# Optimization experiments

Measured on AMD Instinct MI355X. Metric: run time of the kernel, lower is better.

The kernel has to match this reference:

```python
import jax, jax.numpy as jnp
import numpy as np

B, NV, NL, D, H = 32, 512, 256, 1024, 4096


def _ffn(x, w1, b1, w2, b2):
    # torch FFN: linear2(relu(linear1(x))); weights stored as [in, out]
    return jnp.maximum(x @ w1 + b1, 0.0) @ w2 + b2


def setup_inputs() -> dict:
    key = jax.random.key(0)
    ks = jax.random.split(key, 12)
    s_in = 1.0 / np.sqrt(D)
    s_h = 1.0 / np.sqrt(H)
    return {
        "V": jax.random.normal(ks[0], (B, NV, D), jnp.float32),
        "L": jax.random.normal(ks[1], (B, NL, D), jnp.float32),
        "v_mask": jnp.ones((B, NV), jnp.float32),
        "l_mask": jnp.ones((B, NL), jnp.float32),
        "w1_V": jax.random.normal(ks[2], (D, H), jnp.float32) * s_in,
        "b1_V": jnp.zeros((H,), jnp.float32),
        "w2_V": jax.random.normal(ks[3], (H, D), jnp.float32) * s_h,
        "b2_V": jnp.zeros((D,), jnp.float32),
        "w1_L": jax.random.normal(ks[4], (D, H), jnp.float32) * s_in,
        "b1_L": jnp.zeros((H,), jnp.float32),
        "w2_L": jax.random.normal(ks[5], (H, D), jnp.float32) * s_h,
        "b2_L": jnp.zeros((D,), jnp.float32),
    }


def reference(V, L, v_mask, l_mask, w1_V, b1_V, w2_V, b2_V, w1_L, b1_L, w2_L, b2_L):
    # masks are unused in the original forward
    fV_V = _ffn(V, w1_V, b1_V, w2_V, b2_V)  # [B, NV, D] = ffn_V(V)
    fL_L = _ffn(L, w1_L, b1_L, w2_L, b2_L)  # [B, NL, D] = ffn_L(L)
    fL_V = _ffn(V, w1_L, b1_L, w2_L, b2_L)  # [B, NV, D] = ffn_L(V) (as in source)
    scale = 1.0 / jnp.sqrt(jnp.asarray(V.shape[-1], V.dtype))
    A_LV = jnp.einsum('bnd,bmd->bnm', fV_V, fL_L) * scale  # [B, NV, NL]
    A_VV = jnp.einsum('bnd,bmd->bnm', fV_V, fL_V) * scale  # [B, NV, NV]
    A = jnp.concatenate([A_LV, A_VV], axis=-1)             # [B, NV, NL+NV]
    # softmax over dim=1 (rows), as in the source
    attn = jax.nn.softmax(A, axis=1)
    KV = jnp.concatenate([fL_L, fV_V], axis=1)              # [B, NL+NV, D]
    V_next = jnp.einsum('bnk,bkd->bnd', attn, KV)           # [B, NV, D]
    return (A, V_next)
```

## Files before the change

kernel.cpp:

```cpp
#include <hip/hip_runtime.h>
#include <stdint.h>

#define B_   32
#define NV_  512
#define NL_  256
#define D_   1024
#define H_   4096
#define KTOT 768
#define SCALE_ 0.03125f

typedef __attribute__((ext_vector_type(8))) __bf16 bf8_t;
typedef __attribute__((ext_vector_type(4))) float f32x4;

__device__ __forceinline__ unsigned short f2bf(float f) {
    unsigned u = __float_as_uint(f);
    u += 0x7FFFu + ((u >> 16) & 1u);
    return (unsigned short)(u >> 16);
}
__device__ __forceinline__ unsigned pk2(float lo, float hi) {
    return (unsigned)f2bf(lo) | ((unsigned)f2bf(hi) << 16);
}

__device__ __forceinline__ void gl_lds16(const void* g, const void* lds) {
    __builtin_amdgcn_global_load_lds(
        (const __attribute__((address_space(1))) unsigned int*)(uintptr_t)g,
        (__attribute__((address_space(3))) unsigned int*)(unsigned)(uintptr_t)lds,
        16, 0, 0);
}

#define SBAR() asm volatile("s_barrier" ::: "memory")
#define VMC8() asm volatile("s_waitcnt vmcnt(8)" ::: "memory")
#define VMC0() asm volatile("s_waitcnt vmcnt(0)" ::: "memory")
#define LGK0() asm volatile("s_waitcnt lgkmcnt(0)" ::: "memory")

template<int EPI>
__global__ __launch_bounds__(512, 1)
void gemm256(const unsigned short* __restrict__ Ab, long sAz, int lda,
             const unsigned short* __restrict__ Bb, long sBz, int ldb,
             const float* __restrict__ bias, float scale,
             void* __restrict__ Cp, unsigned short* __restrict__ C2p,
             long sCz, int ldc, int K,
             int nx, int ntile, int tpc)
{
    extern __shared__ unsigned char lds[];
    unsigned char* const ldsA = lds;
    unsigned char* const ldsB = lds + 65536;

    const int tid = threadIdx.x;
    const int w = tid >> 6, l = tid & 63;
    const int wr = w >> 2, wc = w & 3;
    const int lrow = l & 15;
    const int kg = l >> 4;

    int t_, z;
    {
        const int bid = blockIdx.x;
        if (tpc > 0) { const int r = bid >> 3, c = bid & 7; z = r / tpc; t_ = c * tpc + r % tpc; }
        else         { z = bid / ntile; t_ = bid - z * ntile; }
    }
    const int n0 = (t_ % nx) * 256, m0 = (t_ / nx) * 256;

    const unsigned short* A  = Ab + (long)z * sAz;
    const unsigned short* Bg = Bb + (long)z * sBz;

    const int srow = tid >> 3;
    const int scol = ((tid & 7) * 8) ^ ((srow & 7) << 3);
    const int ntk = K >> 6;

    const int cs0 = (((l >> 4) * 16)) ^ ((l & 7) << 4);
    const int cs1 = (64 + ((l >> 4) * 16)) ^ ((l & 7) << 4);

    const unsigned short* const sp0 = Bg + (long)(n0 +   0 + srow) * ldb + scol;
    const unsigned short* const sp1 = Bg + (long)(n0 + 128 + srow) * ldb + scol;
    const unsigned short* const sp2 = A  + (long)(m0 +   0 + srow) * lda + scol;
    const unsigned short* const sp3 = A  + (long)(m0 + 128 + srow) * lda + scol;
    const long stB = (long)64 * ldb, stA = (long)64 * lda;

    f32x4 acc[8][4];
#pragma unroll
    for (int i = 0; i < 8; ++i)
#pragma unroll
        for (int j = 0; j < 4; ++j) acc[i][j] = (f32x4){0.f, 0.f, 0.f, 0.f};

#define STG(tau, part) do {                                                   \
        const int buf_ = (tau) & 1;                                           \
        const int kt_ = ((tau) < ntk ? (tau) : ntk - 1);                      \
        if ((part) < 2) {                                                     \
            const unsigned short* s_ = ((part) == 0 ? sp0 : sp1) + (long)kt_ * 64; \
            unsigned char* d_ = ldsB + (buf_ * 2 + (part)) * 16384 + w * 1024;\
            gl_lds16(s_, d_); gl_lds16(s_ + stB, d_ + 8192);                  \
        } else {                                                              \
            const unsigned short* s_ = ((part) == 2 ? sp2 : sp3) + (long)kt_ * 64; \
            unsigned char* d_ = ldsA + (buf_ * 2 + (part) - 2) * 16384 + w * 1024; \
            gl_lds16(s_, d_); gl_lds16(s_ + stA, d_ + 8192);                  \
        } } while (0)

    auto rdA = [&](int buf, int mf, int cs) -> bf8_t {
        return *(const bf8_t*)(ldsA + (buf * 2 + wr) * 16384 + (mf * 16 + lrow) * 128 + cs);
    };
    auto rdB = [&](int buf, int nf, int cs) -> bf8_t {
        return *(const bf8_t*)(ldsB + (buf * 2 + (wc >> 1)) * 16384 +
                               ((wc & 1) * 64 + nf * 16 + lrow) * 128 + cs);
    };

#define MQ(MO, NO, AREG, BREG)                                                \
    _Pragma("unroll")                                                         \
    for (int mf = 0; mf < 4; ++mf)                                            \
    _Pragma("unroll")                                                         \
        for (int nf = 0; nf < 2; ++nf) {                                      \
            acc[(MO)+mf][(NO)+nf] = __builtin_amdgcn_mfma_f32_16x16x32_bf16(  \
                AREG[mf][0], BREG[nf][0], acc[(MO)+mf][(NO)+nf], 0, 0, 0);    \
            acc[(MO)+mf][(NO)+nf] = __builtin_amdgcn_mfma_f32_16x16x32_bf16(  \
                AREG[mf][1], BREG[nf][1], acc[(MO)+mf][(NO)+nf], 0, 0, 0);    \
        }

    STG(0, 0); STG(0, 1); STG(0, 2); STG(0, 3);
    STG(1, 0); STG(1, 1); STG(1, 2); STG(1, 3);
    VMC8();
    SBAR();

    bf8_t a0A[4][2], b0A[2][2];
    bf8_t a0B[4][2], b0B[2][2];
    bf8_t a1r[4][2], b1r[2][2];

#pragma unroll
    for (int mf = 0; mf < 4; ++mf) { a0A[mf][0] = rdA(0, mf, cs0);
                                     a0A[mf][1] = rdA(0, mf, cs1); }
#pragma unroll
    for (int nf = 0; nf < 2; ++nf) { b0A[nf][0] = rdB(0, nf, cs0);
                                     b0A[nf][1] = rdB(0, nf, cs1); }

#define TILEX(BUF, A0C, B0C, A0N, B0N, TAU)                                   \
    __builtin_amdgcn_s_setprio(1);                                            \
    _Pragma("unroll")                                                         \
    for (int mf = 0; mf < 4; ++mf) { a1r[mf][0] = rdA(BUF, mf + 4, cs0);      \
                                     a1r[mf][1] = rdA(BUF, mf + 4, cs1); }    \
    _Pragma("unroll")                                                         \
    for (int nf = 0; nf < 2; ++nf) { b1r[nf][0] = rdB(BUF, nf + 2, cs0);      \
                                     b1r[nf][1] = rdB(BUF, nf + 2, cs1); }    \
    MQ(0, 0, A0C, B0C)                                                        \
    MQ(0, 2, A0C, b1r)                                                        \
    __builtin_amdgcn_s_setprio(0);                                            \
    LGK0();                                                                   \
    SBAR();                                      \
    STG((TAU) + 2, 0); STG((TAU) + 2, 1);                                     \
    STG((TAU) + 2, 2); STG((TAU) + 2, 3);                                     \
    VMC8();                                          \
    SBAR();                                                            \
    __builtin_amdgcn_s_setprio(1);                                            \
    _Pragma("unroll")                                                         \
    for (int mf = 0; mf < 4; ++mf) { A0N[mf][0] = rdA((BUF) ^ 1, mf, cs0);    \
                                     A0N[mf][1] = rdA((BUF) ^ 1, mf, cs1); }  \
    _Pragma("unroll")                                                         \
    for (int nf = 0; nf < 2; ++nf) { B0N[nf][0] = rdB((BUF) ^ 1, nf, cs0);    \
                                     B0N[nf][1] = rdB((BUF) ^ 1, nf, cs1); }  \
    MQ(4, 0, a1r, B0C)                                                        \
    MQ(4, 2, a1r, b1r)                                                        \
    __builtin_amdgcn_s_setprio(0);                                            \
    SBAR();

    for (int t = 0; t < ntk; t += 2) {
        TILEX(0, a0A, b0A, a0B, b0B, t)
        TILEX(1, a0B, b0B, a0A, b0A, t + 1)
    }
#undef TILEX
#undef MQ
#undef STG

    VMC0();
    SBAR();

    if (EPI == 2) {
        float* C = (float*)Cp + (long)z * sCz;
#pragma unroll
        for (int mf = 0; mf < 8; ++mf)
#pragma unroll
            for (int nf = 0; nf < 4; ++nf)
#pragma unroll
                for (int r = 0; r < 4; ++r)
                    C[(long)(m0 + wr * 128 + mf * 16 + kg * 4 + r) * ldc +
                      (n0 + wc * 64 + nf * 16 + lrow)] = acc[mf][nf][r] * scale;
        return;
    }

    unsigned short* C  = (unsigned short*)Cp + (long)z * sCz;
    unsigned short* C2 = C2p ? (C2p + (long)z * sCz) : nullptr;
    unsigned char* const scr = lds + w * 16384;

    float bv[4];
#pragma unroll
    for (int nf = 0; nf < 4; ++nf) bv[nf] = bias[n0 + wc * 64 + nf * 16 + lrow];

#pragma unroll
    for (int p = 0; p < 2; ++p) {
#pragma unroll
        for (int mf = 0; mf < 4; ++mf)
#pragma unroll
            for (int nf = 0; nf < 4; ++nf)
#pragma unroll
                for (int r = 0; r < 4; ++r) {
                    float v = acc[4 * p + mf][nf][r] + bv[nf];
                    if (EPI == 0) v = fmaxf(v, 0.f);
                    *(unsigned short*)(scr + (mf * 16 + kg * 4 + r) * 136 +
                                       (nf * 16 + lrow) * 2) = f2bf(v);
                }
#pragma unroll
        for (int it = 0; it < 8; ++it) {
            const int rr = it * 8 + (l >> 3);
            const uint4 q = *(const uint4*)(scr + rr * 136 + (l & 7) * 16);
            const long off = (long)(m0 + wr * 128 + p * 64 + rr) * ldc +
                             (n0 + wc * 64 + (l & 7) * 8);
            *(uint4*)(C + off) = q;
            if (C2) *(uint4*)(C2 + off) = q;
        }
    }
}

__device__ __forceinline__ void supertile(int nx, int tpc, int& n0, int& m0, int& z)
{
    const int bid = blockIdx.x;
    const int r = bid >> 3, c = bid & 7;
    z = r / tpc;
    const int t = c * tpc + (r % tpc);
    n0 = (t % nx) * 128;
    m0 = (t / nx) * 128;
}

__global__ __launch_bounds__(256)
void col_stats(const float* __restrict__ A, float* __restrict__ Mst, float* __restrict__ RS)
{
    __shared__ float red[4][64];
    const int t = threadIdx.x;
    const int kk = t & 63, ng = t >> 6;
    const int k = blockIdx.x * 64 + kk;
    const int z = blockIdx.y;
    const float* base = A + (long)z * NV_ * KTOT + k;
    float m = -3.0e38f;
    for (int n = ng * 128; n < ng * 128 + 128; ++n) m = fmaxf(m, base[(long)n * KTOT]);
    red[ng][kk] = m;
    __syncthreads();
    m = fmaxf(fmaxf(red[0][kk], red[1][kk]), fmaxf(red[2][kk], red[3][kk]));
    float s = 0.f;
    for (int n = ng * 128; n < ng * 128 + 128; ++n) s += __expf(base[(long)n * KTOT] - m);
    __syncthreads();
    red[ng][kk] = s;
    __syncthreads();
    if (ng == 0) {
        s = red[0][kk] + red[1][kk] + red[2][kk] + red[3][kk];
        Mst[(long)z * KTOT + k] = m;
        RS[(long)z * KTOT + k]  = 1.f / s;
    }
}

__global__ __launch_bounds__(256)
void attn_mfma(const float* __restrict__ Ap, const unsigned short* __restrict__ KVt,
               const float* __restrict__ Mstp, const float* __restrict__ RSp,
               float* __restrict__ Cp, int nx, int tpc)
{
    __shared__ unsigned short As[128 * 32];
    __shared__ unsigned short Bs[128 * 32];

    const int tid = threadIdx.x;
    const int w = tid >> 6, l = tid & 63;
    const int wr = w >> 1, wc = w & 1;
    const int l15 = l & 15, kg = l >> 4;
    const int srow = l >> 2, scol = (l & 3) * 8;
    int n0, m0, z;
    supertile(nx, tpc, n0, m0, z);

    const float* A = Ap + (long)z * NV_ * KTOT;
    const unsigned short* Bg = KVt + (long)z * D_ * KTOT;
    const float* Mz = Mstp + (long)z * KTOT;
    const float* Rz = RSp  + (long)z * KTOT;
    float* C = Cp + (long)z * NV_ * D_;

    const int ar = tid >> 1;
    const int ah = (tid & 1) * 16;

    f32x4 acc[4][4];
#pragma unroll
    for (int m = 0; m < 4; ++m)
#pragma unroll
        for (int n = 0; n < 4; ++n) acc[m][n] = (f32x4){0.f, 0.f, 0.f, 0.f};

    for (int k0 = 0; k0 < KTOT; k0 += 32) {
#pragma unroll
        for (int i = 0; i < 2; ++i) {
            const int g = i * 4 + w;
            gl_lds16(Bg + (long)(n0 + g * 16 + srow) * KTOT + (k0 + scol), &Bs[g * 512]);
        }
        const float* arow = A + (long)(m0 + ar) * KTOT + k0 + ah;
        const float4 x0 = *(const float4*)(arow);
        const float4 x1 = *(const float4*)(arow + 4);
        const float4 x2 = *(const float4*)(arow + 8);
        const float4 x3 = *(const float4*)(arow + 12);
        const float4 ma = *(const float4*)(Mz + k0 + ah);
        const float4 mb = *(const float4*)(Mz + k0 + ah + 4);
        const float4 mc = *(const float4*)(Mz + k0 + ah + 8);
        const float4 md = *(const float4*)(Mz + k0 + ah + 12);
        const float4 ra = *(const float4*)(Rz + k0 + ah);
        const float4 rb = *(const float4*)(Rz + k0 + ah + 4);
        const float4 rc = *(const float4*)(Rz + k0 + ah + 8);
        const float4 rd = *(const float4*)(Rz + k0 + ah + 12);
        const unsigned q0 = pk2(__expf(x0.x - ma.x) * ra.x, __expf(x0.y - ma.y) * ra.y);
        const unsigned q1 = pk2(__expf(x0.z - ma.z) * ra.z, __expf(x0.w - ma.w) * ra.w);
        const unsigned q2 = pk2(__expf(x1.x - mb.x) * rb.x, __expf(x1.y - mb.y) * rb.y);
        const unsigned q3 = pk2(__expf(x1.z - mb.z) * rb.z, __expf(x1.w - mb.w) * rb.w);
        const unsigned q4 = pk2(__expf(x2.x - mc.x) * rc.x, __expf(x2.y - mc.y) * rc.y);
        const unsigned q5 = pk2(__expf(x2.z - mc.z) * rc.z, __expf(x2.w - mc.w) * rc.w);
        const unsigned q6 = pk2(__expf(x3.x - md.x) * rd.x, __expf(x3.y - md.y) * rd.y);
        const unsigned q7 = pk2(__expf(x3.z - md.z) * rd.z, __expf(x3.w - md.w) * rd.w);
        *(uint4*)&As[ar * 32 + ah]     = make_uint4(q0, q1, q2, q3);
        *(uint4*)&As[ar * 32 + ah + 8] = make_uint4(q4, q5, q6, q7);
        __syncthreads();

        bf8_t af[4], bf[4];
#pragma unroll
        for (int m = 0; m < 4; ++m)
            af[m] = *(const bf8_t*)&As[(wr * 64 + m * 16 + l15) * 32 + kg * 8];
#pragma unroll
        for (int n = 0; n < 4; ++n)
            bf[n] = *(const bf8_t*)&Bs[(wc * 64 + n * 16 + l15) * 32 + kg * 8];
#pragma unroll
        for (int m = 0; m < 4; ++m)
#pragma unroll
            for (int n = 0; n < 4; ++n)
                acc[m][n] = __builtin_amdgcn_mfma_f32_16x16x32_bf16(af[m], bf[n], acc[m][n], 0, 0, 0);
        __syncthreads();
    }

    const int orow = wr * 64 + (l >> 4) * 4;
    const int ocol = wc * 64 + l15;
#pragma unroll
    for (int m = 0; m < 4; ++m)
#pragma unroll
        for (int n = 0; n < 4; ++n)
#pragma unroll
            for (int r = 0; r < 4; ++r)
                C[(long)(m0 + orow + m * 16 + r) * D_ + (n0 + ocol + n * 16)] = acc[m][n][r];
}

__global__ __launch_bounds__(256)
void tr2bf_f(const float* __restrict__ src, long sSz, int ldS,
             unsigned short* __restrict__ dst, long sDz, int ldD)
{
    __shared__ unsigned short T[64][65];
    const int t = threadIdx.x;
    const int rr = t >> 2, cc = (t & 3) * 16;
    const int r0 = blockIdx.x * 64, c0 = blockIdx.y * 64, z = blockIdx.z;
    const float* S = src + (long)z * sSz + (long)(r0 + rr) * ldS + c0 + cc;
    const float4 a = *(const float4*)(S);
    const float4 b = *(const float4*)(S + 4);
    const float4 c = *(const float4*)(S + 8);
    const float4 d = *(const float4*)(S + 12);
    unsigned short* Tr = &T[rr][cc];
    Tr[0] = f2bf(a.x); Tr[1] = f2bf(a.y); Tr[2]  = f2bf(a.z); Tr[3]  = f2bf(a.w);
    Tr[4] = f2bf(b.x); Tr[5] = f2bf(b.y); Tr[6]  = f2bf(b.z); Tr[7]  = f2bf(b.w);
    Tr[8] = f2bf(c.x); Tr[9] = f2bf(c.y); Tr[10] = f2bf(c.z); Tr[11] = f2bf(c.w);
    Tr[12] = f2bf(d.x); Tr[13] = f2bf(d.y); Tr[14] = f2bf(d.z); Tr[15] = f2bf(d.w);
    __syncthreads();
    unsigned short v[16];
#pragma unroll
    for (int j = 0; j < 16; ++j) v[j] = T[cc + j][rr];
    unsigned q[8];
#pragma unroll
    for (int j = 0; j < 8; ++j) q[j] = (unsigned)v[2 * j] | ((unsigned)v[2 * j + 1] << 16);
    unsigned short* Dp = dst + (long)z * sDz + (long)(c0 + rr) * ldD + r0 + cc;
    *(uint4*)Dp       = make_uint4(q[0], q[1], q[2], q[3]);
    *(uint4*)(Dp + 8) = make_uint4(q[4], q[5], q[6], q[7]);
}

__global__ __launch_bounds__(256)
void tr2bf_h(const unsigned short* __restrict__ src, long sSz, int ldS,
             unsigned short* __restrict__ dst, long sDz, int ldD)
{
    __shared__ unsigned short T[64][65];
    const int t = threadIdx.x;
    const int rr = t >> 2, cc = (t & 3) * 16;
    const int r0 = blockIdx.x * 64, c0 = blockIdx.y * 64, z = blockIdx.z;
    const unsigned short* S = src + (long)z * sSz + (long)(r0 + rr) * ldS + c0 + cc;
    const uint4 qa = *(const uint4*)(S);
    const uint4 qb = *(const uint4*)(S + 8);
    unsigned short* Tr = &T[rr][cc];
    Tr[0]  = qa.x & 0xFFFF; Tr[1]  = qa.x >> 16; Tr[2]  = qa.y & 0xFFFF; Tr[3]  = qa.y >> 16;
    Tr[4]  = qa.z & 0xFFFF; Tr[5]  = qa.z >> 16; Tr[6]  = qa.w & 0xFFFF; Tr[7]  = qa.w >> 16;
    Tr[8]  = qb.x & 0xFFFF; Tr[9]  = qb.x >> 16; Tr[10] = qb.y & 0xFFFF; Tr[11] = qb.y >> 16;
    Tr[12] = qb.z & 0xFFFF; Tr[13] = qb.z >> 16; Tr[14] = qb.w & 0xFFFF; Tr[15] = qb.w >> 16;
    __syncthreads();
    unsigned short v[16];
#pragma unroll
    for (int j = 0; j < 16; ++j) v[j] = T[cc + j][rr];
    unsigned q[8];
#pragma unroll
    for (int j = 0; j < 8; ++j) q[j] = (unsigned)v[2 * j] | ((unsigned)v[2 * j + 1] << 16);
    unsigned short* Dp = dst + (long)z * sDz + (long)(c0 + rr) * ldD + r0 + cc;
    *(uint4*)Dp       = make_uint4(q[0], q[1], q[2], q[3]);
    *(uint4*)(Dp + 8) = make_uint4(q[4], q[5], q[6], q[7]);
}

__global__ __launch_bounds__(256)
void cvt_bf(const float* __restrict__ src, unsigned short* __restrict__ dst, long n)
{
    const long i = ((long)blockIdx.x * 256 + threadIdx.x) * 8;
    if (i >= n) return;
    const float4 a = *(const float4*)(src + i);
    const float4 b = *(const float4*)(src + i + 4);
    *(uint4*)(dst + i) = make_uint4(pk2(a.x, a.y), pk2(a.z, a.w), pk2(b.x, b.y), pk2(b.z, b.w));
}

extern "C" void kernel_launch(void* const* d_in, const int* in_sizes, int n_in,
                              void* d_out, int out_size, void* d_ws, size_t ws_size,
                              hipStream_t stream)
{
    (void)in_sizes; (void)n_in; (void)out_size;

    const float* V   = (const float*)d_in[0];
    const float* L   = (const float*)d_in[1];
    const float* w1V = (const float*)d_in[4];
    const float* b1V = (const float*)d_in[5];
    const float* w2V = (const float*)d_in[6];
    const float* b2V = (const float*)d_in[7];
    const float* w1L = (const float*)d_in[8];
    const float* b1L = (const float*)d_in[9];
    const float* w2L = (const float*)d_in[10];
    const float* b2L = (const float*)d_in[11];

    float* outA = (float*)d_out;
    float* outV = outA + (size_t)B_ * NV_ * KTOT;

    unsigned short* w1Vt = (unsigned short*)d_ws;
    unsigned short* w2Vt = w1Vt + (size_t)H_ * D_;
    unsigned short* w1Lt = w2Vt + (size_t)D_ * H_;
    unsigned short* w2Lt = w1Lt + (size_t)H_ * D_;
    unsigned short* pool = w2Lt + (size_t)D_ * H_;

    const size_t perb_us = (size_t)NV_ * D_ + (size_t)NL_ * D_ + (size_t)NV_ * H_ +
                           3ul * KTOT * D_;
    const size_t perb_bytes = perb_us * 2 + 2 * (size_t)KTOT * sizeof(float);
    const size_t persist_bytes = (size_t)4 * H_ * D_ * 2;
    const size_t avail = (ws_size > persist_bytes + 256) ? ws_size - persist_bytes - 256 : 0;
    int bc = (int)(avail / perb_bytes);
    if (bc > B_) bc = B_;
    if (bc < 1)  bc = 1;

    unsigned short* Vb   = pool;
    unsigned short* Lb   = Vb   + (size_t)bc * NV_ * D_;
    unsigned short* hid  = Lb   + (size_t)bc * NL_ * D_;
    unsigned short* fCat = hid  + (size_t)bc * NV_ * H_;
    unsigned short* KCat = fCat + (size_t)bc * KTOT * D_;
    unsigned short* KVt  = KCat + (size_t)bc * KTOT * D_;
    float* Mst = (float*)(KVt + (size_t)bc * D_ * KTOT);
    float* RS  = Mst + (size_t)bc * KTOT;

    const dim3 blk(256);
    const dim3 blk5(512);

    {
        auto* f0 = gemm256<0>;
        auto* f1 = gemm256<1>;
        auto* f2 = gemm256<2>;
        hipFuncSetAttribute((const void*)f0, hipFuncAttributeMaxDynamicSharedMemorySize, 131072);
        hipFuncSetAttribute((const void*)f1, hipFuncAttributeMaxDynamicSharedMemorySize, 131072);
        hipFuncSetAttribute((const void*)f2, hipFuncAttributeMaxDynamicSharedMemorySize, 131072);
    }

    tr2bf_f<<<dim3(D_ / 64, H_ / 64, 1), blk, 0, stream>>>(w1V, 0, H_, w1Vt, 0, D_);
    tr2bf_f<<<dim3(H_ / 64, D_ / 64, 1), blk, 0, stream>>>(w2V, 0, D_, w2Vt, 0, H_);
    tr2bf_f<<<dim3(D_ / 64, H_ / 64, 1), blk, 0, stream>>>(w1L, 0, H_, w1Lt, 0, D_);
    tr2bf_f<<<dim3(H_ / 64, D_ / 64, 1), blk, 0, stream>>>(w2L, 0, D_, w2Lt, 0, H_);

    for (int b0 = 0; b0 < B_; b0 += bc) {
        const int cur = (B_ - b0 < bc) ? (B_ - b0) : bc;

        cvt_bf<<<dim3(cur * NV_ * D_ / 2048), blk, 0, stream>>>(
            V + (size_t)b0 * NV_ * D_, Vb, (long)cur * NV_ * D_);
        cvt_bf<<<dim3(cur * NL_ * D_ / 2048), blk, 0, stream>>>(
            L + (size_t)b0 * NL_ * D_, Lb, (long)cur * NL_ * D_);

        #define G256(M, N) dim3((unsigned)(((N) / 256) * ((M) / 256) * cur)), blk5, 131072, stream
        #define P256(M, N) (N) / 256, (((N) / 256) * ((M) / 256)), \
                           ((((N) / 256) * ((M) / 256)) % 8 == 0 ? (((N) / 256) * ((M) / 256)) / 8 : 0)

        gemm256<0><<<G256(NV_, H_)>>>(Vb, (long)NV_ * D_, D_, w1Vt, 0, D_, b1V, 0.f,
                                      hid, nullptr, (long)NV_ * H_, H_, D_, P256(NV_, H_));
        gemm256<1><<<G256(NV_, D_)>>>(hid, (long)NV_ * H_, H_, w2Vt, 0, H_, b2V, 0.f,
                                      KCat + (size_t)NL_ * D_, nullptr,
                                      (long)KTOT * D_, D_, H_, P256(NV_, D_));
        gemm256<0><<<G256(NL_, H_)>>>(Lb, (long)NL_ * D_, D_, w1Lt, 0, D_, b1L, 0.f,
                                      hid, nullptr, (long)NV_ * H_, H_, D_, P256(NL_, H_));
        gemm256<1><<<G256(NL_, D_)>>>(hid, (long)NV_ * H_, H_, w2Lt, 0, H_, b2L, 0.f,
                                      fCat, KCat, (long)KTOT * D_, D_, H_, P256(NL_, D_));
        gemm256<0><<<G256(NV_, H_)>>>(Vb, (long)NV_ * D_, D_, w1Lt, 0, D_, b1L, 0.f,
                                      hid, nullptr, (long)NV_ * H_, H_, D_, P256(NV_, H_));
        gemm256<1><<<G256(NV_, D_)>>>(hid, (long)NV_ * H_, H_, w2Lt, 0, H_, b2L, 0.f,
                                      fCat + (size_t)NL_ * D_, nullptr,
                                      (long)KTOT * D_, D_, H_, P256(NV_, D_));

        gemm256<2><<<G256(NV_, KTOT)>>>(KCat + (size_t)NL_ * D_, (long)KTOT * D_, D_,
                                        fCat, (long)KTOT * D_, D_, nullptr, SCALE_,
                                        outA + (size_t)b0 * NV_ * KTOT, nullptr,
                                        (long)NV_ * KTOT, KTOT, D_, P256(NV_, KTOT));
        #undef G256
        #undef P256

        tr2bf_h<<<dim3(KTOT / 64, D_ / 64, cur), blk, 0, stream>>>(
            KCat, (long)KTOT * D_, D_, KVt, (long)D_ * KTOT, KTOT);

        col_stats<<<dim3(KTOT / 64, cur), blk, 0, stream>>>(
            outA + (size_t)b0 * NV_ * KTOT, Mst, RS);

        attn_mfma<<<dim3((unsigned)((D_ / 128) * (NV_ / 128) * cur)), blk, 0, stream>>>(
            outA + (size_t)b0 * NV_ * KTOT, KVt, Mst, RS,
            outV + (size_t)b0 * NV_ * D_,
            D_ / 128, (D_ / 128) * (NV_ / 128) / 8);
    }
}
```

Before: 961.5 us.

## Switch GEMM to 32x32x16 MFMA and fuse V's two first-layer FFN GEMMs

The 256x256 GEMM kernel now uses 32x32x16 bf16 MFMA instructions with 16-float accumulators instead of 16x16x32. The prefetch pipeline is simplified to a single loop that reads all LDS fragments per k-tile and then issues the MFMAs. Separately, the w1_V and w1_L transposed weights and their biases are laid out contiguously, so the first layer for V under both FFNs runs as one GEMM with N=2H. The goal is fewer MFMA instructions and LDS reads, plus fewer launches with wider grids. In exchange the register pressure changes, the overlap of LDS reads with MFMAs is lost, and the hidden buffer doubles in size, which may reduce the batch chunk.

```diff
diff --git a/kernel.cpp b/kernel.cpp
--- a/kernel.cpp
+++ b/kernel.cpp
@@ -11,6 +11,7 @@
 
 typedef __attribute__((ext_vector_type(8))) __bf16 bf8_t;
 typedef __attribute__((ext_vector_type(4))) float f32x4;
+typedef __attribute__((ext_vector_type(16))) float f32x16;
 
 __device__ __forceinline__ unsigned short f2bf(float f) {
     unsigned u = __float_as_uint(f);
@@ -49,8 +50,8 @@
     const int tid = threadIdx.x;
     const int w = tid >> 6, l = tid & 63;
     const int wr = w >> 2, wc = w & 3;
-    const int lrow = l & 15;
-    const int kg = l >> 4;
+    const int lrow32 = l & 31;
+    const int half = l >> 5;
 
     int t_, z;
     {
@@ -67,8 +68,10 @@
     const int scol = ((tid & 7) * 8) ^ ((srow & 7) << 3);
     const int ntk = K >> 6;
 
-    const int cs0 = (((l >> 4) * 16)) ^ ((l & 7) << 4);
-    const int cs1 = (64 + ((l >> 4) * 16)) ^ ((l & 7) << 4);
+    int cs[4];
+#pragma unroll
+    for (int ks = 0; ks < 4; ++ks)
+        cs[ks] = (ks * 32 + half * 16) ^ ((l & 7) << 4);
 
     const unsigned short* const sp0 = Bg + (long)(n0 +   0 + srow) * ldb + scol;
     const unsigned short* const sp1 = Bg + (long)(n0 + 128 + srow) * ldb + scol;
@@ -76,13 +79,15 @@
     const unsigned short* const sp3 = A  + (long)(m0 + 128 + srow) * lda + scol;
     const long stB = (long)64 * ldb, stA = (long)64 * lda;
 
-    f32x4 acc[8][4];
-#pragma unroll
-    for (int i = 0; i < 8; ++i)
-#pragma unroll
-        for (int j = 0; j < 4; ++j) acc[i][j] = (f32x4){0.f, 0.f, 0.f, 0.f};
-
-#define STG(tau, part) do {                                                   \
+    f32x16 acc[4][2];
+#pragma unroll
+    for (int mt = 0; mt < 4; ++mt)
+#pragma unroll
+        for (int nt = 0; nt < 2; ++nt)
+#pragma unroll
+            for (int e = 0; e < 16; ++e) acc[mt][nt][e] = 0.f;
+
+#define STG1(tau, part) do {                                                  \
         const int buf_ = (tau) & 1;                                           \
         const int kt_ = ((tau) < ntk ? (tau) : ntk - 1);                      \
         if ((part) < 2) {                                                     \
@@ -94,78 +99,52 @@
             unsigned char* d_ = ldsA + (buf_ * 2 + (part) - 2) * 16384 + w * 1024; \
             gl_lds16(s_, d_); gl_lds16(s_ + stA, d_ + 8192);                  \
         } } while (0)
-
-    auto rdA = [&](int buf, int mf, int cs) -> bf8_t {
-        return *(const bf8_t*)(ldsA + (buf * 2 + wr) * 16384 + (mf * 16 + lrow) * 128 + cs);
-    };
-    auto rdB = [&](int buf, int nf, int cs) -> bf8_t {
-        return *(const bf8_t*)(ldsB + (buf * 2 + (wc >> 1)) * 16384 +
-                               ((wc & 1) * 64 + nf * 16 + lrow) * 128 + cs);
-    };
-
-#define MQ(MO, NO, AREG, BREG)                                                \
+#define STG(tau) do { STG1(tau, 0); STG1(tau, 1); STG1(tau, 2); STG1(tau, 3); } while (0)
+
+    bf8_t aR[4][4], bR[2][4];
+
+#define RDS(BUF) do {                                                         \
+        unsigned char* baA = ldsA + ((BUF) * 2 + wr) * 16384;                 \
+        unsigned char* baB = ldsB + ((BUF) * 2 + (wc >> 1)) * 16384;          \
+        _Pragma("unroll")                                                     \
+        for (int mt = 0; mt < 4; ++mt)                                        \
+        _Pragma("unroll")                                                     \
+            for (int ks = 0; ks < 4; ++ks)                                    \
+                aR[mt][ks] = *(const bf8_t*)(baA + (mt * 32 + lrow32) * 128 + cs[ks]); \
+        _Pragma("unroll")                                                     \
+        for (int nt = 0; nt < 2; ++nt)                                        \
+        _Pragma("unroll")                                                     \
+            for (int ks = 0; ks < 4; ++ks)                                    \
+                bR[nt][ks] = *(const bf8_t*)(baB + ((wc & 1) * 64 + nt * 32 + lrow32) * 128 + cs[ks]); \
+    } while (0)
+
+#define MFM()                                                                 \
+    __builtin_amdgcn_s_setprio(1);                                            \
     _Pragma("unroll")                                                         \
-    for (int mf = 0; mf < 4; ++mf)                                            \
+    for (int ks = 0; ks < 4; ++ks)                                            \
     _Pragma("unroll")                                                         \
-        for (int nf = 0; nf < 2; ++nf) {                                      \
-            acc[(MO)+mf][(NO)+nf] = __builtin_amdgcn_mfma_f32_16x16x32_bf16(  \
-                AREG[mf][0], BREG[nf][0], acc[(MO)+mf][(NO)+nf], 0, 0, 0);    \
-            acc[(MO)+mf][(NO)+nf] = __builtin_amdgcn_mfma_f32_16x16x32_bf16(  \
-                AREG[mf][1], BREG[nf][1], acc[(MO)+mf][(NO)+nf], 0, 0, 0);    \
-        }
-
-    STG(0, 0); STG(0, 1); STG(0, 2); STG(0, 3);
-    STG(1, 0); STG(1, 1); STG(1, 2); STG(1, 3);
+        for (int mt = 0; mt < 4; ++mt)                                        \
+        _Pragma("unroll")                                                     \
+            for (int nt = 0; nt < 2; ++nt)                                    \
+                acc[mt][nt] = __builtin_amdgcn_mfma_f32_32x32x16_bf16(        \
+                    aR[mt][ks], bR[nt][ks], acc[mt][nt], 0, 0, 0);            \
+    __builtin_amdgcn_s_setprio(0);
+
+    STG(0); STG(1);
     VMC8();
     SBAR();
 
-    bf8_t a0A[4][2], b0A[2][2];
-    bf8_t a0B[4][2], b0B[2][2];
-    bf8_t a1r[4][2], b1r[2][2];
-
-#pragma unroll
-    for (int mf = 0; mf < 4; ++mf) { a0A[mf][0] = rdA(0, mf, cs0);
-                                     a0A[mf][1] = rdA(0, mf, cs1); }
-#pragma unroll
-    for (int nf = 0; nf < 2; ++nf) { b0A[nf][0] = rdB(0, nf, cs0);
-                                     b0A[nf][1] = rdB(0, nf, cs1); }
-
-#define TILEX(BUF, A0C, B0C, A0N, B0N, TAU)                                   \
-    __builtin_amdgcn_s_setprio(1);                                            \
-    _Pragma("unroll")                                                         \
-    for (int mf = 0; mf < 4; ++mf) { a1r[mf][0] = rdA(BUF, mf + 4, cs0);      \
-                                     a1r[mf][1] = rdA(BUF, mf + 4, cs1); }    \
-    _Pragma("unroll")                                                         \
-    for (int nf = 0; nf < 2; ++nf) { b1r[nf][0] = rdB(BUF, nf + 2, cs0);      \
-                                     b1r[nf][1] = rdB(BUF, nf + 2, cs1); }    \
-    MQ(0, 0, A0C, B0C)                                                        \
-    MQ(0, 2, A0C, b1r)                                                        \
-    __builtin_amdgcn_s_setprio(0);                                            \
-    LGK0();                                                                   \
-    SBAR();                                      \
-    STG((TAU) + 2, 0); STG((TAU) + 2, 1);                                     \
-    STG((TAU) + 2, 2); STG((TAU) + 2, 3);                                     \
-    VMC8();                                          \
-    SBAR();                                                            \
-    __builtin_amdgcn_s_setprio(1);                                            \
-    _Pragma("unroll")                                                         \
-    for (int mf = 0; mf < 4; ++mf) { A0N[mf][0] = rdA((BUF) ^ 1, mf, cs0);    \
-                                     A0N[mf][1] = rdA((BUF) ^ 1, mf, cs1); }  \
-    _Pragma("unroll")                                                         \
-    for (int nf = 0; nf < 2; ++nf) { B0N[nf][0] = rdB((BUF) ^ 1, nf, cs0);    \
-                                     B0N[nf][1] = rdB((BUF) ^ 1, nf, cs1); }  \
-    MQ(4, 0, a1r, B0C)                                                        \
-    MQ(4, 2, a1r, b1r)                                                        \
-    __builtin_amdgcn_s_setprio(0);                                            \
-    SBAR();
-
-    for (int t = 0; t < ntk; t += 2) {
-        TILEX(0, a0A, b0A, a0B, b0B, t)
-        TILEX(1, a0B, b0B, a0A, b0A, t + 1)
-    }
-#undef TILEX
-#undef MQ
+    for (int t = 0; t < ntk; ++t) {
+        RDS(t & 1);
+        LGK0(); SBAR();
+        STG(t + 2);
+        VMC8(); SBAR();
+        MFM()
+    }
+#undef MFM
+#undef RDS
 #undef STG
+#undef STG1
 
     VMC0();
     SBAR();
@@ -173,13 +152,16 @@
     if (EPI == 2) {
         float* C = (float*)Cp + (long)z * sCz;
 #pragma unroll
-        for (int mf = 0; mf < 8; ++mf)
-#pragma unroll
-            for (int nf = 0; nf < 4; ++nf)
-#pragma unroll
-                for (int r = 0; r < 4; ++r)
-                    C[(long)(m0 + wr * 128 + mf * 16 + kg * 4 + r) * ldc +
-                      (n0 + wc * 64 + nf * 16 + lrow)] = acc[mf][nf][r] * scale;
+        for (int mt = 0; mt < 4; ++mt)
+#pragma unroll
+            for (int nt = 0; nt < 2; ++nt)
+#pragma unroll
+                for (int reg = 0; reg < 16; ++reg) {
+                    const int row = m0 + wr * 128 + mt * 32 +
+                                    (reg & 3) + 8 * (reg >> 2) + 4 * half;
+                    const int col = n0 + wc * 64 + nt * 32 + lrow32;
+                    C[(long)row * ldc + col] = acc[mt][nt][reg] * scale;
+                }
         return;
     }
 
@@ -187,22 +169,23 @@
     unsigned short* C2 = C2p ? (C2p + (long)z * sCz) : nullptr;
     unsigned char* const scr = lds + w * 16384;
 
-    float bv[4];
-#pragma unroll
-    for (int nf = 0; nf < 4; ++nf) bv[nf] = bias[n0 + wc * 64 + nf * 16 + lrow];
+    float bv[2];
+#pragma unroll
+    for (int nt = 0; nt < 2; ++nt) bv[nt] = bias[n0 + wc * 64 + nt * 32 + lrow32];
 
 #pragma unroll
     for (int p = 0; p < 2; ++p) {
 #pragma unroll
-        for (int mf = 0; mf < 4; ++mf)
-#pragma unroll
-            for (int nf = 0; nf < 4; ++nf)
-#pragma unroll
-                for (int r = 0; r < 4; ++r) {
-                    float v = acc[4 * p + mf][nf][r] + bv[nf];
+        for (int mh = 0; mh < 2; ++mh)
+#pragma unroll
+            for (int nt = 0; nt < 2; ++nt)
+#pragma unroll
+                for (int reg = 0; reg < 16; ++reg) {
+                    float v = acc[2 * p + mh][nt][reg] + bv[nt];
                     if (EPI == 0) v = fmaxf(v, 0.f);
-                    *(unsigned short*)(scr + (mf * 16 + kg * 4 + r) * 136 +
-                                       (nf * 16 + lrow) * 2) = f2bf(v);
+                    const int sr = mh * 32 + (reg & 3) + 8 * (reg >> 2) + 4 * half;
+                    *(unsigned short*)(scr + sr * 136 +
+                                       (nt * 32 + lrow32) * 2) = f2bf(v);
                 }
 #pragma unroll
         for (int it = 0; it < 8; ++it) {
@@ -428,25 +411,29 @@
     float* outA = (float*)d_out;
     float* outV = outA + (size_t)B_ * NV_ * KTOT;
 
-    unsigned short* w1Vt = (unsigned short*)d_ws;
-    unsigned short* w2Vt = w1Vt + (size_t)H_ * D_;
-    unsigned short* w1Lt = w2Vt + (size_t)D_ * H_;
-    unsigned short* w2Lt = w1Lt + (size_t)H_ * D_;
+    unsigned short* w1cat = (unsigned short*)d_ws;
+    unsigned short* w1Vt = w1cat;
+    unsigned short* w1Lt = w1cat + (size_t)H_ * D_;
+    unsigned short* w2Vt = w1Lt + (size_t)H_ * D_;
+    unsigned short* w2Lt = w2Vt + (size_t)D_ * H_;
     unsigned short* pool = w2Lt + (size_t)D_ * H_;
 
-    const size_t perb_us = (size_t)NV_ * D_ + (size_t)NL_ * D_ + (size_t)NV_ * H_ +
-                           3ul * KTOT * D_;
+    float* b1cat = (float*)(pool);
+    unsigned short* pool2 = (unsigned short*)(b1cat + 2 * H_);
+
+    const size_t perb_us = (size_t)NV_ * D_ + (size_t)NL_ * D_ +
+                           (size_t)NV_ * 2 * H_ + 3ul * KTOT * D_;
     const size_t perb_bytes = perb_us * 2 + 2 * (size_t)KTOT * sizeof(float);
-    const size_t persist_bytes = (size_t)4 * H_ * D_ * 2;
+    const size_t persist_bytes = (size_t)4 * H_ * D_ * 2 + 2 * H_ * 4 + 256;
     const size_t avail = (ws_size > persist_bytes + 256) ? ws_size - persist_bytes - 256 : 0;
     int bc = (int)(avail / perb_bytes);
     if (bc > B_) bc = B_;
     if (bc < 1)  bc = 1;
 
-    unsigned short* Vb   = pool;
+    unsigned short* Vb   = pool2;
     unsigned short* Lb   = Vb   + (size_t)bc * NV_ * D_;
-    unsigned short* hid  = Lb   + (size_t)bc * NL_ * D_;
-    unsigned short* fCat = hid  + (size_t)bc * NV_ * H_;
+    unsigned short* hidc = Lb   + (size_t)bc * NL_ * D_;
+    unsigned short* fCat = hidc + (size_t)bc * NV_ * 2 * H_;
     unsigned short* KCat = fCat + (size_t)bc * KTOT * D_;
     unsigned short* KVt  = KCat + (size_t)bc * KTOT * D_;
     float* Mst = (float*)(KVt + (size_t)bc * D_ * KTOT);
@@ -465,9 +452,11 @@
     }
 
     tr2bf_f<<<dim3(D_ / 64, H_ / 64, 1), blk, 0, stream>>>(w1V, 0, H_, w1Vt, 0, D_);
+    tr2bf_f<<<dim3(D_ / 64, H_ / 64, 1), blk, 0, stream>>>(w1L, 0, H_, w1Lt, 0, D_);
     tr2bf_f<<<dim3(H_ / 64, D_ / 64, 1), blk, 0, stream>>>(w2V, 0, D_, w2Vt, 0, H_);
-    tr2bf_f<<<dim3(D_ / 64, H_ / 64, 1), blk, 0, stream>>>(w1L, 0, H_, w1Lt, 0, D_);
     tr2bf_f<<<dim3(H_ / 64, D_ / 64, 1), blk, 0, stream>>>(w2L, 0, D_, w2Lt, 0, H_);
+    hipMemcpyAsync(b1cat, b1V, H_ * sizeof(float), hipMemcpyDeviceToDevice, stream);
+    hipMemcpyAsync(b1cat + H_, b1L, H_ * sizeof(float), hipMemcpyDeviceToDevice, stream);
 
     for (int b0 = 0; b0 < B_; b0 += bc) {
         const int cur = (B_ - b0 < bc) ? (B_ - b0) : bc;
@@ -481,20 +470,20 @@
         #define P256(M, N) (N) / 256, (((N) / 256) * ((M) / 256)), \
                            ((((N) / 256) * ((M) / 256)) % 8 == 0 ? (((N) / 256) * ((M) / 256)) / 8 : 0)
 
-        gemm256<0><<<G256(NV_, H_)>>>(Vb, (long)NV_ * D_, D_, w1Vt, 0, D_, b1V, 0.f,
-                                      hid, nullptr, (long)NV_ * H_, H_, D_, P256(NV_, H_));
-        gemm256<1><<<G256(NV_, D_)>>>(hid, (long)NV_ * H_, H_, w2Vt, 0, H_, b2V, 0.f,
+        gemm256<0><<<G256(NV_, 2 * H_)>>>(Vb, (long)NV_ * D_, D_, w1cat, 0, D_, b1cat, 0.f,
+                                          hidc, nullptr, (long)NV_ * 2 * H_, 2 * H_, D_,
+                                          P256(NV_, 2 * H_));
+        gemm256<1><<<G256(NV_, D_)>>>(hidc, (long)NV_ * 2 * H_, 2 * H_, w2Vt, 0, H_, b2V, 0.f,
                                       KCat + (size_t)NL_ * D_, nullptr,
                                       (long)KTOT * D_, D_, H_, P256(NV_, D_));
-        gemm256<0><<<G256(NL_, H_)>>>(Lb, (long)NL_ * D_, D_, w1Lt, 0, D_, b1L, 0.f,
-                                      hid, nullptr, (long)NV_ * H_, H_, D_, P256(NL_, H_));
-        gemm256<1><<<G256(NL_, D_)>>>(hid, (long)NV_ * H_, H_, w2Lt, 0, H_, b2L, 0.f,
-                                      fCat, KCat, (long)KTOT * D_, D_, H_, P256(NL_, D_));
-        gemm256<0><<<G256(NV_, H_)>>>(Vb, (long)NV_ * D_, D_, w1Lt, 0, D_, b1L, 0.f,
-                                      hid, nullptr, (long)NV_ * H_, H_, D_, P256(NV_, H_));
-        gemm256<1><<<G256(NV_, D_)>>>(hid, (long)NV_ * H_, H_, w2Lt, 0, H_, b2L, 0.f,
+        gemm256<1><<<G256(NV_, D_)>>>(hidc + H_, (long)NV_ * 2 * H_, 2 * H_, w2Lt, 0, H_, b2L, 0.f,
                                       fCat + (size_t)NL_ * D_, nullptr,
                                       (long)KTOT * D_, D_, H_, P256(NV_, D_));
+        gemm256<0><<<G256(NL_, H_)>>>(Lb, (long)NL_ * D_, D_, w1Lt, 0, D_, b1L, 0.f,
+                                      hidc, nullptr, (long)NV_ * 2 * H_, H_, D_,
+                                      P256(NL_, H_));
+        gemm256<1><<<G256(NL_, D_)>>>(hidc, (long)NV_ * 2 * H_, H_, w2Lt, 0, H_, b2L, 0.f,
+                                      fCat, KCat, (long)KTOT * D_, D_, H_, P256(NL_, D_));
 
         gemm256<2><<<G256(NV_, KTOT)>>>(KCat + (size_t)NL_ * D_, (long)KTOT * D_, D_,
                                         fCat, (long)KTOT * D_, D_, nullptr, SCALE_,
```

Measured after the change: 1.604 ms. 66.8% more time.
